# Performance work log

Hardware: AMD Instinct MI355X
Metric: run time of the kernel (lower is better)

The kernel has to match this reference:

```python
import jax, jax.numpy as jnp
import numpy as np
import math

B, S, DIM, H, HD = 2, 2048, 2048, 16, 128


def _rotary(t, cos, sin):
    # t: [B, S, H, HD]; cos/sin: [S, HD//2]
    tr = t.reshape(*t.shape[:-1], HD // 2, 2)
    t_re, t_im = tr[..., 0], tr[..., 1]
    c = cos[None, :, None, :]
    s = sin[None, :, None, :]
    o_re = t_re * c - t_im * s
    o_im = t_re * s + t_im * c
    out = jnp.stack([o_re, o_im], axis=-1)
    return out.reshape(t.shape)


def setup_inputs() -> dict:
    key = jax.random.key(0)
    ks = jax.random.split(key, 6)
    x = jax.random.normal(ks[0], (B, S, DIM), dtype=jnp.float32)
    # rotary frequencies (base 10000), matching complex freqs_cis = exp(i * t * freq)
    inv_freq = 1.0 / (10000.0 ** (np.arange(0, HD, 2, dtype=np.float32) / HD))
    t = np.arange(S, dtype=np.float32)
    ang = np.outer(t, inv_freq)  # [S, HD//2]
    freqs_cos = jnp.asarray(np.cos(ang), dtype=jnp.float32)
    freqs_sin = jnp.asarray(np.sin(ang), dtype=jnp.float32)
    # causal boolean mask [1,1,S,S]
    mask = jnp.tril(jnp.ones((S, S), dtype=bool))[None, None]
    scale = 0.02
    qw = jax.random.normal(ks[1], (DIM, H * HD), dtype=jnp.float32) * scale
    kw = jax.random.normal(ks[2], (DIM, H * HD), dtype=jnp.float32) * scale
    vw = jax.random.normal(ks[3], (DIM, H * HD), dtype=jnp.float32) * scale
    ow = jax.random.normal(ks[4], (H * HD, DIM), dtype=jnp.float32) * scale
    return {"x": x, "freqs_cos": freqs_cos, "freqs_sin": freqs_sin, "mask": mask,
            "qw": qw, "kw": kw, "vw": vw, "ow": ow}


def reference(x, freqs_cos, freqs_sin, mask, qw, kw, vw, ow):
    bsz, slen, _ = x.shape
    q = (x @ qw).reshape(bsz, slen, H, HD)
    k = (x @ kw).reshape(bsz, slen, H, HD)
    v = (x @ vw).reshape(bsz, slen, H, HD)
    q = _rotary(q, freqs_cos[:slen], freqs_sin[:slen])
    k = _rotary(k, freqs_cos[:slen], freqs_sin[:slen])
    # [B, H, S, HD]
    q = q.transpose(0, 2, 1, 3)
    k = k.transpose(0, 2, 1, 3)
    v = v.transpose(0, 2, 1, 3)
    scale = 1.0 / math.sqrt(HD)
    scores = jnp.einsum('bhqd,bhkd->bhqk', q, k) * scale
    neg_inf = jnp.finfo(scores.dtype).min
    scores = jnp.where(mask, scores, neg_inf)
    attn_w = jax.nn.softmax(scores, axis=-1)
    attn = jnp.einsum('bhqk,bhkd->bhqd', attn_w, v)
    attn = attn.transpose(0, 2, 1, 3).reshape(bsz, slen, H * HD)
    out = attn @ ow
    return (out, attn_w)
```

## Files before the change

### kernel.cpp

```cpp
#include <hip/hip_runtime.h>
#include <stdint.h>

#define S 2048
#define DIMM 2048
#define NH 16
#define HD 128
#define NB 2
#define M4 4096

typedef unsigned short u16;
typedef unsigned int u32;
typedef __attribute__((ext_vector_type(8))) short short8;
typedef __attribute__((ext_vector_type(4))) float f32x4;

__device__ __forceinline__ u16 f2bf(float f) {
  union { float f; u32 u; } v; v.f = f;
  u32 u = v.u + 0x7fffu + ((v.u >> 16) & 1u);
  return (u16)(u >> 16);
}
__device__ __forceinline__ float bf2f(u16 b) {
  union { u32 u; float f; } v; v.u = ((u32)b) << 16;
  return v.f;
}
__device__ __forceinline__ u32 cvt_pk_bf16(float lo, float hi) {
  u32 r; asm("v_cvt_pk_bf16_f32 %0, %1, %2" : "=v"(r) : "v"(lo), "v"(hi)); return r;
}
__device__ __forceinline__ void gl_lds16(const void* g, void* l) {
  __builtin_amdgcn_global_load_lds((const __attribute__((address_space(1))) void*)g,
                                   (__attribute__((address_space(3))) void*)l, 16, 0, 0);
}
#define MFMA16(a, b, c) __builtin_amdgcn_mfma_f32_16x16x32_bf16(a, b, c, 0, 0, 0)

__global__ __launch_bounds__(256) void k_prep(const float* __restrict__ x, u16* __restrict__ xb,
                                              const float* __restrict__ w0, const float* __restrict__ w1,
                                              const float* __restrict__ w2, const float* __restrict__ w3,
                                              u16* __restrict__ t0, u16* __restrict__ t1,
                                              u16* __restrict__ t2, u16* __restrict__ t3) {
  int zi = blockIdx.z;
  int tid = threadIdx.x;
  if (zi >= 4) {
    int bid = (zi - 4) * 1024 + blockIdx.y * 32 + blockIdx.x;
    int i = (bid * 256 + tid) * 8;
    float4 a = *(const float4*)&x[i];
    float4 b = *(const float4*)&x[i + 4];
    uint4 o;
    o.x = (u32)f2bf(a.x) | ((u32)f2bf(a.y) << 16);
    o.y = (u32)f2bf(a.z) | ((u32)f2bf(a.w) << 16);
    o.z = (u32)f2bf(b.x) | ((u32)f2bf(b.y) << 16);
    o.w = (u32)f2bf(b.z) | ((u32)f2bf(b.w) << 16);
    *(uint4*)&xb[i] = o;
    return;
  }
  __shared__ u16 t[64][72];
  const float* w = (zi == 0) ? w0 : (zi == 1) ? w1 : (zi == 2) ? w2 : w3;
  u16* wt = (zi == 0) ? t0 : (zi == 1) ? t1 : (zi == 2) ? t2 : t3;
  int k0 = blockIdx.y * 64, n0 = blockIdx.x * 64;
  int r0 = tid >> 4, c4 = (tid & 15) * 4;
#pragma unroll
  for (int p = 0; p < 4; ++p) {
    int r = r0 + p * 16;
    float4 v = *(const float4*)&w[(size_t)(k0 + r) * DIMM + n0 + c4];
    t[c4 + 0][r] = f2bf(v.x); t[c4 + 1][r] = f2bf(v.y);
    t[c4 + 2][r] = f2bf(v.z); t[c4 + 3][r] = f2bf(v.w);
  }
  __syncthreads();
#pragma unroll
  for (int p = 0; p < 2; ++p) {
    int cc = tid + p * 256;
    int rn = cc >> 3, ck = (cc & 7) * 8;
    *(uint4*)&wt[(size_t)(n0 + rn) * DIMM + k0 + ck] = *(const uint4*)&t[rn][ck];
  }
}

__device__ __forceinline__ void gemm128_core(const u16* __restrict__ A, const u16* __restrict__ Bt,
                                             int m0, int n0, int Kd, u16* lA, u16* lB,
                                             f32x4 acc[4][4]) {
  int tid = threadIdx.x;
  int lane = tid & 63;
  int wid = tid >> 6;
  int wm = wid >> 1, wn = wid & 1;
  int c0 = tid, c1 = tid + 256;
  int a_r0 = c0 >> 2, a_k0 = (c0 & 3) * 8;
  int a_r1 = c1 >> 2, a_k1 = (c1 & 3) * 8;
  int ln = lane & 15, sub = lane >> 4;
  for (int kt = 0; kt < Kd; kt += 32) {
    gl_lds16(&A[(size_t)(m0 + a_r0) * Kd + kt + a_k0], &lA[c0 * 8]);
    gl_lds16(&A[(size_t)(m0 + a_r1) * Kd + kt + a_k1], &lA[c1 * 8]);
    gl_lds16(&Bt[(size_t)(n0 + a_r0) * Kd + kt + a_k0], &lB[c0 * 8]);
    gl_lds16(&Bt[(size_t)(n0 + a_r1) * Kd + kt + a_k1], &lB[c1 * 8]);
    __syncthreads();
    short8 af[4], bf[4];
#pragma unroll
    for (int mf = 0; mf < 4; ++mf)
      af[mf] = *(const short8*)&lA[(wm * 64 + mf * 16 + ln) * 32 + sub * 8];
#pragma unroll
    for (int nf = 0; nf < 4; ++nf)
      bf[nf] = *(const short8*)&lB[(wn * 64 + nf * 16 + ln) * 32 + sub * 8];
#pragma unroll
    for (int mf = 0; mf < 4; ++mf)
#pragma unroll
      for (int nf = 0; nf < 4; ++nf)
        acc[mf][nf] = MFMA16(af[mf], bf[nf], acc[mf][nf]);
    __syncthreads();
  }
}

__global__ __launch_bounds__(256) void k_gemm_qkv(const u16* __restrict__ xb,
                                                  const u16* __restrict__ qwT, const u16* __restrict__ kwT,
                                                  const u16* __restrict__ vwT,
                                                  const float* __restrict__ fc, const float* __restrict__ fs,
                                                  u16* __restrict__ qws, u16* __restrict__ kws,
                                                  u16* __restrict__ vtws) {
  __shared__ u16 lA[128 * 32], lB[128 * 32];
  int f = blockIdx.y * 48 + blockIdx.x;
  int fp = (f & 7) * 192 + (f >> 3);
  int bx = fp % 48, byy = fp / 48;

  int region = bx >> 4;
  const u16* Bt = (region == 0) ? qwT : ((region == 1) ? kwT : vwT);
  int n0 = (bx & 15) * 128;
  int m0 = byy * 128;
  f32x4 acc[4][4];
  f32x4 z4 = {0.f, 0.f, 0.f, 0.f};
#pragma unroll
  for (int i = 0; i < 4; ++i)
#pragma unroll
    for (int j = 0; j < 4; ++j) acc[i][j] = z4;
  gemm128_core(xb, Bt, m0, n0, DIMM, lA, lB, acc);
  int lane = threadIdx.x & 63, wid = threadIdx.x >> 6;
  int wm = wid >> 1, wn = wid & 1;
  int ln = lane & 15, sub = lane >> 4;
  if (region == 2) {
#pragma unroll
    for (int mf = 0; mf < 4; ++mf)
#pragma unroll
      for (int nf = 0; nf < 4; ++nf) {
        int m = m0 + wm * 64 + mf * 16 + sub * 4;
        int nl = n0 + wn * 64 + nf * 16 + ln;
        int b = m >> 11, s = m & 2047;
        int h = nl >> 7, d = nl & 127;
        u32 w0 = cvt_pk_bf16(acc[mf][nf][0], acc[mf][nf][1]);
        u32 w1 = cvt_pk_bf16(acc[mf][nf][2], acc[mf][nf][3]);
        uint2 pw = {w0, w1};
        *(uint2*)&vtws[((size_t)((b << 4) + h) * HD + d) * S + s] = pw;
      }
  } else {
    u16* dst = (region == 0) ? qws : kws;
#pragma unroll
    for (int mf = 0; mf < 4; ++mf)
#pragma unroll
      for (int nf = 0; nf < 4; ++nf) {
        int mbase = m0 + wm * 64 + mf * 16 + sub * 4;
        int nl = n0 + wn * 64 + nf * 16 + ln;
        int h = nl >> 7, d = nl & 127;
        int pi = d >> 1;
#pragma unroll
        for (int r = 0; r < 4; ++r) {
          int m = mbase + r;
          int b = m >> 11, s = m & 2047;
          float c = fc[s * 64 + pi];
          float sn = fs[s * 64 + pi];
          float v = acc[mf][nf][r];
          float prt = __shfl_xor(v, 1);
          float o = (ln & 1) ? (prt * sn + v * c) : (v * c - prt * sn);
          float o2 = __shfl_xor(o, 1);
          if (!(ln & 1)) {
            u32 opk = cvt_pk_bf16(o, o2);
            *(u32*)&dst[((size_t)((b << 4) + h) * S + s) * HD + d] = opk;
          }
        }
      }
  }
}

__global__ __launch_bounds__(256, 4) void k_attn(const u16* __restrict__ qws, const u16* __restrict__ kws,
                                                 const u16* __restrict__ vtws,
                                                 float* __restrict__ aw_all, u16* __restrict__ att) {
  __shared__ u16 lK[2][32 * 128];
  __shared__ u16 lV[2][128 * 32];
  __shared__ u16 lP[64 * 32];

  int f = blockIdx.x;
  int x = f & 7;
  int j = f >> 3;
  int cu = j & 31;
  int u = j >> 5;
  int by = 4 * x + u;
  int c2 = (u & 2) ? ((cu + 16) & 31) : cu;
  int qt = (u & 1) ? (31 - c2) : c2;
  int b = by >> 4, h = by & 15;
  const u16* qb = qws + (size_t)by * S * HD;
  const u16* kb = kws + (size_t)by * S * HD;
  const u16* vb = vtws + (size_t)by * HD * S;
  float* aw = aw_all + (size_t)by * S * S;
  int tid = threadIdx.x, lane = tid & 63, w = tid >> 6;
  int sub = lane >> 4, ln = lane & 15;
  int l7 = ln & 7, l3 = ln & 3;
  int q0 = qt * 64;
  int qrow = w * 16 + ln;
  int nkt = 2 * qt + 2;
  const float SC = 0.08838834764831845f * 1.4426950408889634f;

  auto stageK = [&](int kt, int bs) {
#pragma unroll
    for (int i = 0; i < 2; ++i) {
      int c = tid + i * 256;
      int row = c >> 4, p = c & 15;
      gl_lds16(&kb[(size_t)(kt * 32 + row) * HD + ((p ^ (row & 7)) << 3)], &lK[bs][c * 8]);
    }
  };
  auto stageV = [&](int kt, int bs) {
#pragma unroll
    for (int i = 0; i < 2; ++i) {
      int c = tid + i * 256;
      int row = c >> 2, p = c & 3;
      gl_lds16(&vb[(size_t)row * S + kt * 32 + ((p ^ (row & 3)) << 3)], &lV[bs][c * 8]);
    }
  };

  u16* lVlin = &lV[0][0];
#pragma unroll
  for (int i = 0; i < 4; ++i) {
    int c = tid + i * 256;
    int row = c >> 4, p = c & 15;
    gl_lds16(&qb[(size_t)(q0 + row) * HD + ((p ^ (row & 7)) << 3)], &lVlin[c * 8]);
  }
  stageK(0, 0);
  __syncthreads();

  short8 qf[4];
#pragma unroll
  for (int ks = 0; ks < 4; ++ks)
    qf[ks] = *(const short8*)&lVlin[qrow * 128 + (((ks * 4 + sub) ^ l7) << 3)];

  float ts = 0.f;
  for (int kt = 0; kt < nkt; ++kt) {
    int cur = kt & 1;
    if (kt + 1 < nkt) stageK(kt + 1, cur ^ 1);
    f32x4 sacc[2];
#pragma unroll
    for (int nf = 0; nf < 2; ++nf) sacc[nf] = f32x4{0.f, 0.f, 0.f, 0.f};
    __builtin_amdgcn_s_setprio(1);
#pragma unroll
    for (int nf = 0; nf < 2; ++nf) {
      int krow = nf * 16 + ln;
#pragma unroll
      for (int ks = 0; ks < 4; ++ks) {
        short8 kf = *(const short8*)&lK[cur][krow * 128 + (((ks * 4 + sub) ^ l7) << 3)];
        sacc[nf] = MFMA16(kf, qf[ks], sacc[nf]);
      }
    }
    __builtin_amdgcn_s_setprio(0);
    bool msk = (kt >= 2 * qt);
#pragma unroll
    for (int nf = 0; nf < 2; ++nf)
#pragma unroll
      for (int r = 0; r < 4; ++r) {
        float zz = sacc[nf][r] * SC;
        bool dead = msk && (kt * 32 + nf * 16 + sub * 4 + r > q0 + qrow);
        if (!dead) ts += exp2f(zz);
      }
    __syncthreads();
  }
  ts += __shfl_xor(ts, 16);
  ts += __shfl_xor(ts, 32);
  float mb = __log2f(ts);

  f32x4 oacc[8];
#pragma unroll
  for (int i = 0; i < 8; ++i) oacc[i] = f32x4{0.f, 0.f, 0.f, 0.f};
  stageK(nkt - 1, 0);
  stageV(nkt - 1, 0);
  __syncthreads();
  for (int it = 0; it < nkt; ++it) {
    int kt = nkt - 1 - it;
    int cur = it & 1;
    if (it + 1 < nkt) { stageK(kt - 1, cur ^ 1); stageV(kt - 1, cur ^ 1); }
    f32x4 sacc[2];
#pragma unroll
    for (int nf = 0; nf < 2; ++nf) sacc[nf] = f32x4{0.f, 0.f, 0.f, 0.f};
    __builtin_amdgcn_s_setprio(1);
#pragma unroll
    for (int nf = 0; nf < 2; ++nf) {
      int krow = nf * 16 + ln;
#pragma unroll
      for (int ks = 0; ks < 4; ++ks) {
        short8 kf = *(const short8*)&lK[cur][krow * 128 + (((ks * 4 + sub) ^ l7) << 3)];
        sacc[nf] = MFMA16(kf, qf[ks], sacc[nf]);
      }
    }
    __builtin_amdgcn_s_setprio(0);
    bool msk = (kt >= 2 * qt);
#pragma unroll
    for (int nf = 0; nf < 2; ++nf) {
      float p0 = exp2f(sacc[nf][0] * SC - mb);
      float p1 = exp2f(sacc[nf][1] * SC - mb);
      float p2 = exp2f(sacc[nf][2] * SC - mb);
      float p3 = exp2f(sacc[nf][3] * SC - mb);
      if (msk) {
        int base = kt * 32 + nf * 16 + sub * 4 - (q0 + qrow);
        if (base + 0 > 0) p0 = 0.f;
        if (base + 1 > 0) p1 = 0.f;
        if (base + 2 > 0) p2 = 0.f;
        if (base + 3 > 0) p3 = 0.f;
      }
      f32x4 pv = {p0, p1, p2, p3};
      __builtin_nontemporal_store(pv, (f32x4*)&aw[(size_t)(q0 + qrow) * S + kt * 32 + nf * 16 + sub * 4]);
      u32 w0 = cvt_pk_bf16(p0, p1);
      u32 w1 = cvt_pk_bf16(p2, p3);
      uint2 pw = {w0, w1};
      int c16 = (2 * nf + (sub >> 1)) ^ l3;
      *(uint2*)&lP[qrow * 32 + (c16 << 3) + ((sub & 1) << 2)] = pw;
    }
    short8 pa = *(const short8*)&lP[qrow * 32 + ((sub ^ l3) << 3)];
    __builtin_amdgcn_s_setprio(1);
#pragma unroll
    for (int nf2 = 0; nf2 < 8; ++nf2) {
      int drow = nf2 * 16 + ln;
      short8 vv = *(const short8*)&lV[cur][drow * 32 + ((sub ^ (drow & 3)) << 3)];
      oacc[nf2] = MFMA16(vv, pa, oacc[nf2]);
    }
    __builtin_amdgcn_s_setprio(0);
    __syncthreads();
  }

#pragma unroll
  for (int nf2 = 0; nf2 < 8; ++nf2) {
    u32 w0 = cvt_pk_bf16(oacc[nf2][0], oacc[nf2][1]);
    u32 w1 = cvt_pk_bf16(oacc[nf2][2], oacc[nf2][3]);
    uint2 ow2 = {w0, w1};
    *(uint2*)&att[(size_t)(b * S + q0 + qrow) * (NH * HD) + h * 128 + nf2 * 16 + sub * 4] = ow2;
  }

  {
    f32x4 zf = {0.f, 0.f, 0.f, 0.f};
    for (int kt2 = qt + 1; kt2 < 32; ++kt2) {
      float* base = aw + (size_t)q0 * S + kt2 * 64;
#pragma unroll
      for (int i = 0; i < 4; ++i) {
        int c = i * 256 + tid;
        int row = c >> 4, col = (c & 15) * 4;
        __builtin_nontemporal_store(zf, (f32x4*)&base[(size_t)row * S + col]);
      }
    }
  }
}

__global__ __launch_bounds__(256) void k_gemm_out(const u16* __restrict__ att, const u16* __restrict__ owT,
                                                  float* __restrict__ out) {
  __shared__ u16 lA[128 * 32], lB[128 * 32];
  int f = blockIdx.y * 16 + blockIdx.x;
  int fp = (f & 7) * 64 + (f >> 3);
  int n0 = (fp & 15) * 128, m0 = (fp >> 4) * 128;
  f32x4 acc[4][4];
  f32x4 z4 = {0.f, 0.f, 0.f, 0.f};
#pragma unroll
  for (int i = 0; i < 4; ++i)
#pragma unroll
    for (int j = 0; j < 4; ++j) acc[i][j] = z4;
  gemm128_core(att, owT, m0, n0, DIMM, lA, lB, acc);
  int lane = threadIdx.x & 63, wid = threadIdx.x >> 6;
  int wm = wid >> 1, wn = wid & 1;
  int ln = lane & 15, sub = lane >> 4;
#pragma unroll
  for (int mf = 0; mf < 4; ++mf)
#pragma unroll
    for (int nf = 0; nf < 4; ++nf)
#pragma unroll
      for (int r = 0; r < 4; ++r) {
        int m = m0 + wm * 64 + mf * 16 + sub * 4 + r;
        int nl = n0 + wn * 64 + nf * 16 + ln;
        out[(size_t)m * DIMM + nl] = acc[mf][nf][r];
      }
}

extern "C" void kernel_launch(void* const* d_in, const int* in_sizes, int n_in,
                              void* d_out, int out_size, void* d_ws, size_t ws_size,
                              hipStream_t stream) {
  const float* x  = (const float*)d_in[0];
  const float* fc = (const float*)d_in[1];
  const float* fs = (const float*)d_in[2];
  const float* qw = (const float*)d_in[4];
  const float* kw = (const float*)d_in[5];
  const float* vw = (const float*)d_in[6];
  const float* ow = (const float*)d_in[7];
  float* out = (float*)d_out;
  float* aw  = out + (size_t)M4 * DIMM;

  char* wsb = (char*)d_ws;
  u16* xb   = (u16*)(wsb);
  u16* qwT  = (u16*)(wsb + (size_t)16 * 1024 * 1024);
  u16* kwT  = (u16*)(wsb + (size_t)24 * 1024 * 1024);
  u16* vwT  = (u16*)(wsb + (size_t)32 * 1024 * 1024);
  u16* owT  = (u16*)(wsb + (size_t)40 * 1024 * 1024);
  u16* qws  = (u16*)(wsb + (size_t)48 * 1024 * 1024);
  u16* kws  = (u16*)(wsb + (size_t)64 * 1024 * 1024);
  u16* vtws = (u16*)(wsb + (size_t)80 * 1024 * 1024);
  u16* att  = (u16*)(wsb + (size_t)96 * 1024 * 1024);

  k_prep<<<dim3(32, 32, 8), 256, 0, stream>>>(x, xb, qw, kw, vw, ow, qwT, kwT, vwT, owT);
  k_gemm_qkv<<<dim3(48, 32), 256, 0, stream>>>(xb, qwT, kwT, vwT, fc, fs, qws, kws, vtws);
  k_attn<<<1024, 256, 0, stream>>>(qws, kws, vtws, aw, att);
  k_gemm_out<<<dim3(16, 32), 256, 0, stream>>>(att, owT, out);
}
```

Measured before the change: 377.9 us.

## Double GEMM K-tile to 64 with XOR-swizzled LDS and relax attention loop barrier

The shared GEMM core now stages a 64-wide K slice per iteration instead of 32, halving the number of barrier pairs over the K loop. Its LDS layout is XOR-swizzled to avoid bank conflicts on the wider rows. In the attention PV loop, the trailing full __syncthreads is replaced by a partial vmcnt wait plus s_barrier, and it is skipped on the last iteration. This lets the prefetch loads overlap further, at the risk of races if the vmcnt count does not match the outstanding loads.

```diff
diff --git a/kernel.cpp b/kernel.cpp
--- a/kernel.cpp
+++ b/kernel.cpp
@@ -72,35 +72,39 @@
   }
 }
 
-__device__ __forceinline__ void gemm128_core(const u16* __restrict__ A, const u16* __restrict__ Bt,
-                                             int m0, int n0, int Kd, u16* lA, u16* lB,
-                                             f32x4 acc[4][4]) {
+__device__ __forceinline__ void gemm128_core64(const u16* __restrict__ A, const u16* __restrict__ Bt,
+                                               int m0, int n0, int Kd, u16* lA, u16* lB,
+                                               f32x4 acc[4][4]) {
   int tid = threadIdx.x;
   int lane = tid & 63;
   int wid = tid >> 6;
   int wm = wid >> 1, wn = wid & 1;
-  int c0 = tid, c1 = tid + 256;
-  int a_r0 = c0 >> 2, a_k0 = (c0 & 3) * 8;
-  int a_r1 = c1 >> 2, a_k1 = (c1 & 3) * 8;
   int ln = lane & 15, sub = lane >> 4;
-  for (int kt = 0; kt < Kd; kt += 32) {
-    gl_lds16(&A[(size_t)(m0 + a_r0) * Kd + kt + a_k0], &lA[c0 * 8]);
-    gl_lds16(&A[(size_t)(m0 + a_r1) * Kd + kt + a_k1], &lA[c1 * 8]);
-    gl_lds16(&Bt[(size_t)(n0 + a_r0) * Kd + kt + a_k0], &lB[c0 * 8]);
-    gl_lds16(&Bt[(size_t)(n0 + a_r1) * Kd + kt + a_k1], &lB[c1 * 8]);
+  int l7 = ln & 7;
+  for (int kt = 0; kt < Kd; kt += 64) {
+#pragma unroll
+    for (int i = 0; i < 4; ++i) {
+      int c = tid + i * 256;
+      int row = c >> 3, p = c & 7;
+      gl_lds16(&A[(size_t)(m0 + row) * Kd + kt + ((p ^ (row & 7)) << 3)], &lA[c * 8]);
+      gl_lds16(&Bt[(size_t)(n0 + row) * Kd + kt + ((p ^ (row & 7)) << 3)], &lB[c * 8]);
+    }
     __syncthreads();
-    short8 af[4], bf[4];
-#pragma unroll
-    for (int mf = 0; mf < 4; ++mf)
-      af[mf] = *(const short8*)&lA[(wm * 64 + mf * 16 + ln) * 32 + sub * 8];
-#pragma unroll
-    for (int nf = 0; nf < 4; ++nf)
-      bf[nf] = *(const short8*)&lB[(wn * 64 + nf * 16 + ln) * 32 + sub * 8];
-#pragma unroll
-    for (int mf = 0; mf < 4; ++mf)
+#pragma unroll
+    for (int ks = 0; ks < 2; ++ks) {
+      short8 af[4], bf[4];
+#pragma unroll
+      for (int mf = 0; mf < 4; ++mf)
+        af[mf] = *(const short8*)&lA[(wm * 64 + mf * 16 + ln) * 64 + (((ks * 4 + sub) ^ l7) << 3)];
 #pragma unroll
       for (int nf = 0; nf < 4; ++nf)
-        acc[mf][nf] = MFMA16(af[mf], bf[nf], acc[mf][nf]);
+        bf[nf] = *(const short8*)&lB[(wn * 64 + nf * 16 + ln) * 64 + (((ks * 4 + sub) ^ l7) << 3)];
+#pragma unroll
+      for (int mf = 0; mf < 4; ++mf)
+#pragma unroll
+        for (int nf = 0; nf < 4; ++nf)
+          acc[mf][nf] = MFMA16(af[mf], bf[nf], acc[mf][nf]);
+    }
     __syncthreads();
   }
 }
@@ -111,7 +115,7 @@
                                                   const float* __restrict__ fc, const float* __restrict__ fs,
                                                   u16* __restrict__ qws, u16* __restrict__ kws,
                                                   u16* __restrict__ vtws) {
-  __shared__ u16 lA[128 * 32], lB[128 * 32];
+  __shared__ u16 lA[128 * 64], lB[128 * 64];
   int f = blockIdx.y * 48 + blockIdx.x;
   int fp = (f & 7) * 192 + (f >> 3);
   int bx = fp % 48, byy = fp / 48;
@@ -126,7 +130,7 @@
   for (int i = 0; i < 4; ++i)
 #pragma unroll
     for (int j = 0; j < 4; ++j) acc[i][j] = z4;
-  gemm128_core(xb, Bt, m0, n0, DIMM, lA, lB, acc);
+  gemm128_core64(xb, Bt, m0, n0, DIMM, lA, lB, acc);
   int lane = threadIdx.x & 63, wid = threadIdx.x >> 6;
   int wm = wid >> 1, wn = wid & 1;
   int ln = lane & 15, sub = lane >> 4;
@@ -275,7 +279,8 @@
   for (int it = 0; it < nkt; ++it) {
     int kt = nkt - 1 - it;
     int cur = it & 1;
-    if (it + 1 < nkt) { stageK(kt - 1, cur ^ 1); stageV(kt - 1, cur ^ 1); }
+    bool pf = (it + 1 < nkt);
+    if (pf) { stageK(kt - 1, cur ^ 1); stageV(kt - 1, cur ^ 1); }
     f32x4 sacc[2];
 #pragma unroll
     for (int nf = 0; nf < 2; ++nf) sacc[nf] = f32x4{0.f, 0.f, 0.f, 0.f};
@@ -321,7 +326,11 @@
       oacc[nf2] = MFMA16(vv, pa, oacc[nf2]);
     }
     __builtin_amdgcn_s_setprio(0);
-    __syncthreads();
+    if (pf) {
+      asm volatile("s_waitcnt vmcnt(2)" ::: "memory");
+      __builtin_amdgcn_s_barrier();
+      __builtin_amdgcn_sched_barrier(0);
+    }
   }
 
 #pragma unroll
@@ -348,7 +357,7 @@
 
 __global__ __launch_bounds__(256) void k_gemm_out(const u16* __restrict__ att, const u16* __restrict__ owT,
                                                   float* __restrict__ out) {
-  __shared__ u16 lA[128 * 32], lB[128 * 32];
+  __shared__ u16 lA[128 * 64], lB[128 * 64];
   int f = blockIdx.y * 16 + blockIdx.x;
   int fp = (f & 7) * 64 + (f >> 3);
   int n0 = (fp & 15) * 128, m0 = (fp >> 4) * 128;
@@ -358,7 +367,7 @@
   for (int i = 0; i < 4; ++i)
 #pragma unroll
     for (int j = 0; j < 4; ++j) acc[i][j] = z4;
-  gemm128_core(att, owT, m0, n0, DIMM, lA, lB, acc);
+  gemm128_core64(att, owT, m0, n0, DIMM, lA, lB, acc);
   int lane = threadIdx.x & 63, wid = threadIdx.x >> 6;
   int wm = wid >> 1, wn = wid & 1;
   int ln = lane & 15, sub = lane >> 4;
```

New measurement: 391.8 us. 3.7% more time.
